# Kernel optimization log

Measured on AMD Instinct MI355X. Metric: run time of the kernel, lower is better.

## Reference

```python
import jax, jax.numpy as jnp
import numpy as np

NB, NX, NU, NY, NQ = 8192, 512, 128, 128, 256


def setup_inputs() -> dict:
    key = jax.random.key(0)
    ks = jax.random.split(key, 13)
    x = jax.random.normal(ks[0], (NB, NX), dtype=jnp.float32)
    u = jax.random.normal(ks[1], (NB, NU), dtype=jnp.float32)
    C1 = jax.random.normal(ks[2], (NQ, NX), dtype=jnp.float32) / np.sqrt(NX).astype(np.float32)
    D11 = jax.random.normal(ks[3], (NQ, NQ), dtype=jnp.float32) / np.sqrt(NQ).astype(np.float32)
    D12 = jax.random.normal(ks[4], (NQ, NU), dtype=jnp.float32) / np.sqrt(NU).astype(np.float32)
    # Lambda is a positive-diagonal matrix (only Lambda[k,k] is used in the recurrence)
    lam_diag = jax.random.uniform(ks[5], (NQ,), dtype=jnp.float32, minval=0.5, maxval=1.5)
    Lambda = jnp.diag(lam_diag)
    bv = 0.1 * jax.random.normal(ks[6], (NQ, 1), dtype=jnp.float32)
    # E must be invertible (set by the REN wrapper in the original code)
    E = jnp.eye(NX, dtype=jnp.float32) + 0.05 * jax.random.normal(ks[7], (NX, NX), dtype=jnp.float32) / np.sqrt(NX).astype(np.float32)
    F = jax.random.normal(ks[8], (NX, NX), dtype=jnp.float32) / np.sqrt(NX).astype(np.float32)
    B1 = jax.random.normal(ks[9], (NX, NQ), dtype=jnp.float32) / np.sqrt(NQ).astype(np.float32)
    B2 = jax.random.normal(ks[10], (NX, NU), dtype=jnp.float32) / np.sqrt(NU).astype(np.float32)
    C2 = jax.random.normal(ks[11], (NY, NX), dtype=jnp.float32) / np.sqrt(NX).astype(np.float32)
    D21 = jax.random.normal(ks[12], (NY, NQ), dtype=jnp.float32) / np.sqrt(NQ).astype(np.float32)
    return {"x": x, "u": u, "C1": C1, "D11": D11, "D12": D12, "Lambda": Lambda,
            "bv": bv, "E": E, "F": F, "B1": B1, "B2": B2, "C2": C2, "D21": D21}


def _solve_w(x, u, C1, D11, D12, lam_diag, bv):
    # Loop-invariant part of v_k: x @ C1[k]^T + u @ D12[k]^T + bv[k]
    base = x @ C1.T + u @ D12.T + bv[:, 0][None, :]  # (nb, nq)
    nb = x.shape[0]
    nq = C1.shape[0]

    def step(w, k):
        # w columns >= k are still zero, matching the torch loop semantics
        v = (base[:, k] + w @ D11[k]) / lam_diag[k]  # (nb,)
        w = w.at[:, k].set(jnp.tanh(v))
        return w, None

    w0 = jnp.zeros((nb, nq), dtype=x.dtype)
    w, _ = jax.lax.scan(step, w0, jnp.arange(nq))
    return w


def reference(x, u, C1, D11, D12, Lambda, bv, E, F, B1, B2, C2, D21):
    lam_diag = jnp.diagonal(Lambda)
    w = _solve_w(x, u, C1, D11, D12, lam_diag, bv)
    # E^{-1} @ M computed via solve (same math as torch.inverse(E) @ M)
    EinvF = jnp.linalg.solve(E, F)
    EinvB1 = jnp.linalg.solve(E, B1)
    EinvB2 = jnp.linalg.solve(E, B2)
    dx = x @ EinvF.T + w @ EinvB1.T + u @ EinvB2.T
    y = x @ C2.T + w @ D21.T
    return (dx, y)
```

## Files before the change

### kernel.cpp

```cpp
#include <hip/hip_runtime.h>

typedef unsigned short u16;
typedef unsigned int   u32;
typedef __attribute__((ext_vector_type(8))) __bf16 bf16x8;
typedef __attribute__((ext_vector_type(4))) float  f32x4;
typedef __attribute__((ext_vector_type(4))) u16    u16x4;
typedef __attribute__((ext_vector_type(4))) u32    u32x4;

#define DEV __device__ __forceinline__

DEV u16 f2b(float f){ union{float f;u32 u;}a; a.f=f; u32 r=a.u + 0x7FFFu + ((a.u>>16)&1u); return (u16)(r>>16); }
DEV float b2f(u16 h){ union{u32 u;float f;}a; a.u=((u32)h)<<16; return a.f; }

typedef __attribute__((address_space(1))) void* gp1;
typedef __attribute__((address_space(3))) void* lp3;
DEV void gl16(const void* g, void* l){
  __builtin_amdgcn_global_load_lds((gp1)g, (lp3)l, 16, 0, 0);
}

__global__ __launch_bounds__(256) void k_prepc(
    const float* __restrict__ x,  const float* __restrict__ u,
    const float* __restrict__ C1, const float* __restrict__ D11,
    const float* __restrict__ D12, const float* __restrict__ Lam,
    const float* __restrict__ E,  const float* __restrict__ F,
    const float* __restrict__ B1, const float* __restrict__ B2,
    const float* __restrict__ C2, const float* __restrict__ D21,
    u16* Ebf, u16* Y0, u16* Z0, u16* McatT, u16* Qt, u16* Rt,
    float* invLam, u16* Ddg2, float* Dt16, u16* P)
{
  if (blockIdx.x < 704) {
    __shared__ float t[32][33];
    int bid = blockIdx.x;
    const int tx = threadIdx.x & 31, ty = threadIdx.x >> 5;
    const float* src; u16* dst; int srcC, nA, task;
    if (bid < 256)      { task = 0; src = E;   srcC = 512; dst = Z0;    nA = 16; }
    else if (bid < 512) { task = 1; src = F;   srcC = 512; dst = McatT; nA = 16; bid -= 256; }
    else if (bid < 640) { task = 2; src = B1;  srcC = 256; dst = McatT + (size_t)640 * 512; nA = 8;  bid -= 512; }
    else                { task = 3; src = B2;  srcC = 128; dst = McatT + (size_t)512 * 512; nA = 4;  bid -= 640; }
    const int a0 = (bid % nA) * 32;
    const int b0 = (bid / nA) * 32;
    #pragma unroll
    for (int k = 0; k < 4; k++) {
      int srow = b0 + ty + 8 * k;
      t[ty + 8 * k][tx] = src[(size_t)srow * srcC + a0 + tx];
    }
    __syncthreads();
    #pragma unroll
    for (int k = 0; k < 4; k++) {
      int drow = a0 + ty + 8 * k, dcol = b0 + tx;
      float v = t[tx][ty + 8 * k];
      if (task == 0) v = ((drow == dcol) ? 2.f : 0.f) - v;
      dst[(size_t)drow * 512 + dcol] = f2b(v);
    }
    return;
  }
  int idx = (blockIdx.x - 704) * 256 + threadIdx.x;
  if (idx < 262144) {
    int i = idx >> 9, j = idx & 511;
    float e = E[idx];
    Ebf[idx] = f2b(e);
    float dij = (i == j) ? 2.f : 0.f;
    Y0[idx] = f2b(dij - e);
    return;
  }
  idx -= 262144;
  if (idx < 114688) {
    int j = idx / 896, k = idx - j * 896;
    float v = (k < 512) ? C2[j * 512 + k]
              : (k < 640 ? 0.f : D21[j * 256 + (k - 640)]);
    Qt[(size_t)(512 + j) * 896 + k] = f2b(v);
    return;
  }
  idx -= 114688;
  if (idx < 163840) {
    int n = idx / 640, k = idx - n * 640;
    float v = (k < 512) ? C1[n * 512 + k] : D12[n * 128 + (k - 512)];
    Rt[idx] = f2b(v);
    return;
  }
  idx -= 163840;
  if (idx < 256) { invLam[idx] = 1.f / Lam[idx * 257]; return; }
  idx -= 256;
  if (idx < 65536) {
    int sb = idx >> 13, t = (idx >> 9) & 15, l = (idx >> 3) & 63, j = idx & 7;
    int r = l & 15, g = l >> 4;
    int n = t * 16 + r, k = sb * 32 + g * 8 + j;
    Ddg2[idx] = f2b(D11[n * 256 + k] * (1.f / Lam[n * 257]));
    return;
  }
  idx -= 65536;
  if (idx < 4096) {
    int T = idx >> 8, k2 = (idx >> 4) & 15, n2 = idx & 15;
    float v = 0.f;
    if (n2 > k2) {
      int n = T * 16 + n2;
      v = D11[n * 256 + T * 16 + k2] * (1.f / Lam[n * 257]);
    }
    Dt16[idx] = v;
    return;
  }
  idx -= 4096;
  {
    int b = idx / 160, t = idx - b * 160;
    f32x4 s; u16* dst;
    if (t < 128) { s = *(const f32x4*)(x + (size_t)b * 512 + t * 4); dst = P + (size_t)b * 896 + t * 4; }
    else         { s = *(const f32x4*)(u + (size_t)b * 128 + (t - 128) * 4); dst = P + (size_t)b * 896 + 512 + (t - 128) * 4; }
    u16x4 o; o.x = f2b(s.x); o.y = f2b(s.y); o.z = f2b(s.z); o.w = f2b(s.w);
    *(u16x4*)dst = o;
  }
}

struct GemmArgs {
  const u16* A; const u16* B; int K; int lda; int ldb;
  u16* outB; int ldB;
  u16* outBT;
  const u16* Yprev;
};

template<int EPI>
DEV void gemm64_body(const GemmArgs& g, int bm, int bn, u16* As, u16* Bs)
{
  const int tid = threadIdx.x;
  const int l = tid & 63, w = tid >> 6;
  const int K = g.K;
  const size_t rowbA = (size_t)g.lda * 2, rowbB = (size_t)g.ldb * 2;
  const char* Ab = (const char*)g.A + (size_t)bm * 64 * rowbA;
  const char* Bb = (const char*)g.B + (size_t)bn * 64 * rowbB;
  const int o = tid * 16;
  const int r0 = o >> 6;
  const int cs = (((o >> 4) ^ r0) & 3) << 4;
  char* AsB = (char*)As; char* BsB = (char*)Bs;
  const int wm = w >> 1, wn = w & 1;
  const int lr = l & 15, lk = l >> 4;
  const int slot = ((lk ^ lr) & 3) << 4;

  f32x4 acc[2][2];
  const f32x4 zz = {0.f, 0.f, 0.f, 0.f};
  acc[0][0] = zz; acc[0][1] = zz; acc[1][0] = zz; acc[1][1] = zz;

  for (int k0 = 0; k0 < K; k0 += 32) {
    gl16(Ab + (size_t)r0 * rowbA + k0 * 2 + cs, AsB + o);
    gl16(Bb + (size_t)r0 * rowbB + k0 * 2 + cs, BsB + o);
    __syncthreads();
    bf16x8 af[2], bfv[2];
    #pragma unroll
    for (int mi = 0; mi < 2; mi++)
      af[mi] = *(const bf16x8*)(AsB + (wm * 32 + mi * 16 + lr) * 64 + slot);
    #pragma unroll
    for (int ni = 0; ni < 2; ni++)
      bfv[ni] = *(const bf16x8*)(BsB + (wn * 32 + ni * 16 + lr) * 64 + slot);
    #pragma unroll
    for (int mi = 0; mi < 2; mi++)
      #pragma unroll
      for (int ni = 0; ni < 2; ni++)
        acc[mi][ni] = __builtin_amdgcn_mfma_f32_16x16x32_bf16(af[mi], bfv[ni], acc[mi][ni], 0, 0, 0);
    __syncthreads();
  }

  #pragma unroll
  for (int mi = 0; mi < 2; mi++) {
    #pragma unroll
    for (int ni = 0; ni < 2; ni++) {
      const int row0 = bm * 64 + wm * 32 + mi * 16 + lk * 4;
      const int col  = bn * 64 + wn * 32 + ni * 16 + lr;
      if (EPI == 2) {
        #pragma unroll
        for (int r = 0; r < 4; r++)
          g.outB[(size_t)(row0 + r) * g.ldB + col] = f2b(acc[mi][ni][r]);
      } else if (EPI == 3) {
        #pragma unroll
        for (int r = 0; r < 4; r++)
          g.outBT[(size_t)col * 512 + (row0 + r)] = f2b(acc[mi][ni][r]);
      }
    }
  }
}

template<int EPI>
DEV void gemm64h_body(const GemmArgs& g, int bm, int bn, u16* As, u16* Bs)
{
  const int tid = threadIdx.x;
  const int l = tid & 63, w = tid >> 6;
  const int K = g.K;
  const size_t rowbA = (size_t)g.lda * 2, rowbB = (size_t)g.ldb * 2;
  const char* Ab = (const char*)g.A + (size_t)bm * 64 * rowbA;
  const char* Bb = (const char*)g.B + (size_t)bn * 64 * rowbB;
  const int o1 = tid * 16, o2 = o1 + 2048;
  const int rA1 = o1 >> 6, rA2 = o2 >> 6;
  const int cs1 = (((o1 >> 4) ^ rA1) & 3) << 4;
  const int cs2 = (((o2 >> 4) ^ rA2) & 3) << 4;
  char* AsB = (char*)As; char* BsB = (char*)Bs;
  const int lr = l & 15, lk = l >> 4;
  const int slot = ((lk ^ lr) & 3) << 4;

  f32x4 acc[2][4];
  const f32x4 zz = {0.f, 0.f, 0.f, 0.f};
  #pragma unroll
  for (int i = 0; i < 2; i++)
    #pragma unroll
    for (int j = 0; j < 4; j++) acc[i][j] = zz;

  for (int k0 = 0; k0 < K; k0 += 32) {
    gl16(Ab + (size_t)rA1 * rowbA + k0 * 2 + cs1, AsB + o1);
    gl16(Ab + (size_t)rA2 * rowbA + k0 * 2 + cs2, AsB + o2);
    gl16(Bb + (size_t)rA1 * rowbB + k0 * 2 + cs1, BsB + o1);
    gl16(Bb + (size_t)rA2 * rowbB + k0 * 2 + cs2, BsB + o2);
    __syncthreads();
    bf16x8 af[2], bfv[4];
    #pragma unroll
    for (int mi = 0; mi < 2; mi++)
      af[mi] = *(const bf16x8*)(AsB + (w * 32 + mi * 16 + lr) * 64 + slot);
    #pragma unroll
    for (int ni = 0; ni < 4; ni++)
      bfv[ni] = *(const bf16x8*)(BsB + (ni * 16 + lr) * 64 + slot);
    #pragma unroll
    for (int mi = 0; mi < 2; mi++)
      #pragma unroll
      for (int ni = 0; ni < 4; ni++)
        acc[mi][ni] = __builtin_amdgcn_mfma_f32_16x16x32_bf16(af[mi], bfv[ni], acc[mi][ni], 0, 0, 0);
    __syncthreads();
  }

  #pragma unroll
  for (int mi = 0; mi < 2; mi++) {
    #pragma unroll
    for (int ni = 0; ni < 4; ni++) {
      const int row0 = bm * 64 + w * 32 + mi * 16 + lk * 4;
      const int col  = bn * 64 + ni * 16 + lr;
      if (EPI == 4) {
        #pragma unroll
        for (int r = 0; r < 4; r++) {
          int row = row0 + r;
          float d = 2.f * b2f(g.Yprev[row * 512 + col]) - acc[mi][ni][r];
          g.outB[(size_t)row * 512 + col] = f2b(d);
        }
      }
    }
  }
}

template<int EPI>
__global__ __launch_bounds__(256) void gemm64(GemmArgs g)
{
  __shared__ __align__(16) u16 As[64 * 32];
  __shared__ __align__(16) u16 Bs[64 * 32];
  gemm64_body<EPI>(g, blockIdx.y, blockIdx.x, As, Bs);
}

__global__ __launch_bounds__(256) void gemm_b2(
    const u16* __restrict__ A, const u16* __restrict__ B, float* __restrict__ outF,
    const float* __restrict__ bv, const float* __restrict__ iLam, GemmArgs ga)
{
  __shared__ __align__(16) u16 As[64 * 32];
  __shared__ __align__(16) u16 Bs[128 * 32];
  if (blockIdx.x >= 256) {
    int q = blockIdx.x - 256;
    gemm64_body<3>(ga, q >> 3, q & 7, As, Bs);
    return;
  }
  const int bid = blockIdx.x;
  const int wg = (bid & 7) * 32 + (bid >> 3);
  const int bm = wg >> 1, bn = wg & 1;
  const int tid = threadIdx.x;
  const int l = tid & 63, w = tid >> 6;
  const size_t rowbA = 896 * 2, rowbB = 640 * 2;
  const char* Ab = (const char*)A + (size_t)bm * 64 * rowbA;
  const char* Bb = (const char*)B + (size_t)bn * 128 * rowbB;
  const int o = tid * 16, o2 = o + 4096;
  const int rA = o >> 6;
  const int csA = (((o >> 4) ^ rA) & 3) << 4;
  const int rB2 = o2 >> 6;
  const int csB2 = (((o2 >> 4) ^ rB2) & 3) << 4;
  char* AsB = (char*)As; char* BsB = (char*)Bs;
  const int wm = w >> 1, wn = w & 1;
  const int lr = l & 15, lk = l >> 4;
  const int slot = ((lk ^ lr) & 3) << 4;

  f32x4 acc[2][4];
  const f32x4 zz = {0.f, 0.f, 0.f, 0.f};
  #pragma unroll
  for (int i = 0; i < 2; i++)
    #pragma unroll
    for (int j = 0; j < 4; j++) acc[i][j] = zz;

  for (int k0 = 0; k0 < 640; k0 += 32) {
    gl16(Ab + (size_t)rA * rowbA + k0 * 2 + csA, AsB + o);
    gl16(Bb + (size_t)rA * rowbB + k0 * 2 + csA, BsB + o);
    gl16(Bb + (size_t)rB2 * rowbB + k0 * 2 + csB2, BsB + o2);
    __syncthreads();
    bf16x8 af[2], bfv[4];
    #pragma unroll
    for (int mi = 0; mi < 2; mi++)
      af[mi] = *(const bf16x8*)(AsB + (wm * 32 + mi * 16 + lr) * 64 + slot);
    #pragma unroll
    for (int ni = 0; ni < 4; ni++)
      bfv[ni] = *(const bf16x8*)(BsB + (wn * 64 + ni * 16 + lr) * 64 + slot);
    #pragma unroll
    for (int mi = 0; mi < 2; mi++)
      #pragma unroll
      for (int ni = 0; ni < 4; ni++)
        acc[mi][ni] = __builtin_amdgcn_mfma_f32_16x16x32_bf16(af[mi], bfv[ni], acc[mi][ni], 0, 0, 0);
    __syncthreads();
  }

  #pragma unroll
  for (int mi = 0; mi < 2; mi++) {
    #pragma unroll
    for (int ni = 0; ni < 4; ni++) {
      const int row0 = bm * 64 + wm * 32 + mi * 16 + lk * 4;
      const int col  = bn * 128 + wn * 64 + ni * 16 + lr;
      const float bvc = bv[col], il = iLam[col];
      #pragma unroll
      for (int r = 0; r < 4; r++)
        outF[(size_t)(row0 + r) * 256 + col] = (acc[mi][ni][r] + bvc) * il;
    }
  }
}

__global__ __launch_bounds__(256) void gemm_f(
    const u16* __restrict__ A, const u16* __restrict__ B,
    float* __restrict__ dxOut, float* __restrict__ yOut)
{
  __shared__ __align__(16) u16 As[128 * 32];
  __shared__ __align__(16) u16 Bs[128 * 32];
  const int bid = blockIdx.x;
  const int wg = (bid & 7) * 40 + (bid >> 3);
  const int bm = wg / 5, bn = wg - bm * 5;
  const int tid = threadIdx.x;
  const int l = tid & 63, w = tid >> 6;
  const size_t rowb = 896 * 2;
  const char* Ab = (const char*)A + (size_t)bm * 128 * rowb;
  const char* Bb = (const char*)B + (size_t)bn * 128 * rowb;
  const int o1 = tid * 16, o2 = o1 + 4096;
  const int r1 = o1 >> 6, r2 = o2 >> 6;
  const int c1 = (((o1 >> 4) ^ r1) & 3) << 4;
  const int c2 = (((o2 >> 4) ^ r2) & 3) << 4;
  char* AsB = (char*)As; char* BsB = (char*)Bs;
  const int wm = w >> 1, wn = w & 1;
  const int lr = l & 15, lk = l >> 4;
  const int slot = ((lk ^ lr) & 3) << 4;

  f32x4 acc[4][4];
  const f32x4 zz = {0.f, 0.f, 0.f, 0.f};
  #pragma unroll
  for (int i = 0; i < 4; i++)
    #pragma unroll
    for (int j = 0; j < 4; j++) acc[i][j] = zz;

  for (int k0 = 0; k0 < 896; k0 += 32) {
    gl16(Ab + (size_t)r1 * rowb + k0 * 2 + c1, AsB + o1);
    gl16(Ab + (size_t)r2 * rowb + k0 * 2 + c2, AsB + o2);
    gl16(Bb + (size_t)r1 * rowb + k0 * 2 + c1, BsB + o1);
    gl16(Bb + (size_t)r2 * rowb + k0 * 2 + c2, BsB + o2);
    __syncthreads();
    bf16x8 af[4], bfv[4];
    #pragma unroll
    for (int mi = 0; mi < 4; mi++)
      af[mi] = *(const bf16x8*)(AsB + (wm * 64 + mi * 16 + lr) * 64 + slot);
    #pragma unroll
    for (int ni = 0; ni < 4; ni++)
      bfv[ni] = *(const bf16x8*)(BsB + (wn * 64 + ni * 16 + lr) * 64 + slot);
    #pragma unroll
    for (int mi = 0; mi < 4; mi++)
      #pragma unroll
      for (int ni = 0; ni < 4; ni++)
        acc[mi][ni] = __builtin_amdgcn_mfma_f32_16x16x32_bf16(af[mi], bfv[ni], acc[mi][ni], 0, 0, 0);
    __syncthreads();
  }

  #pragma unroll
  for (int mi = 0; mi < 4; mi++) {
    #pragma unroll
    for (int ni = 0; ni < 4; ni++) {
      const int row0 = bm * 128 + wm * 64 + mi * 16 + lk * 4;
      const int col  = bn * 128 + wn * 64 + ni * 16 + lr;
      #pragma unroll
      for (int r = 0; r < 4; r++) {
        float v = acc[mi][ni][r];
        if (col < 512) dxOut[(size_t)(row0 + r) * 512 + col] = v;
        else           yOut[(size_t)(row0 + r) * 128 + (col - 512)] = v;
      }
    }
  }
}

__global__ __launch_bounds__(128) void k_solve_a(
    const float* __restrict__ base2, const u16* __restrict__ Ddg2,
    const float* __restrict__ Dt16, u16* __restrict__ P, GemmArgs ga)
{
  __shared__ __align__(16) char DdL[2][16384];
  __shared__ __align__(16) float DtL[4096];
  __shared__ __align__(16) float tb[2][16][40];

  if (blockIdx.x >= 256) {
    int q = blockIdx.x - 256;
    gemm64h_body<4>(ga, q >> 3, q & 7, (u16*)&DdL[0][0], (u16*)&DdL[0][4096]);
    return;
  }

  const int tid = threadIdx.x, l = tid & 63, w = tid >> 6;
  const int r = l & 15, g = l >> 4;
  const int row = blockIdx.x * 32 + w * 16 + r;

  const char* DtG = (const char*)Dt16;
  #pragma unroll
  for (int i = 0; i < 8; i++)
    gl16(DtG + i * 2048 + tid * 16, (char*)DtL + i * 2048 + tid * 16);
  const char* DgG = (const char*)Ddg2;
  #pragma unroll
  for (int i = 0; i < 8; i++)
    gl16(DgG + i * 2048 + tid * 16, DdL[0] + i * 2048 + tid * 16);

  f32x4 st[16];
  const float* bp = base2 + (size_t)row * 256 + g * 4;
  #pragma unroll
  for (int t = 0; t < 16; t++) st[t] = *(const f32x4*)(bp + t * 16);

  u32x4 pkA[8];
  float* tbr = &tb[w][r][0];
  __syncthreads();

  #pragma unroll
  for (int sb = 0; sb < 8; sb++) {
    if (sb < 7) {
      #pragma unroll
      for (int i = 0; i < 8; i++)
        gl16(DgG + (sb + 1) * 16384 + i * 2048 + tid * 16,
             DdL[(sb + 1) & 1] + i * 2048 + tid * 16);
    }
    float ws[8];
    #pragma unroll
    for (int i = 0; i < 8; i++) ws[i] = 0.f;
    f32x4 vv[4];

    *(f32x4*)(tbr + g * 4) = st[2 * sb];
    vv[0] = *(const f32x4*)(tbr);      vv[1] = *(const f32x4*)(tbr + 4);
    vv[2] = *(const f32x4*)(tbr + 8);  vv[3] = *(const f32x4*)(tbr + 12);
    {
      const float* dt = DtL + (2 * sb) * 256;
      #pragma unroll
      for (int k2 = 0; k2 < 16; k2++) {
        float v = vv[k2 >> 2][k2 & 3];
        float ex = __expf(2.f * v);
        float wv = 1.f - 2.f * __fdividef(1.f, ex + 1.f);
        if (g == (k2 >> 3)) ws[k2 & 7] = wv;
        #pragma unroll
        for (int j = k2 >> 2; j < 4; j++)
          vv[j] += wv * *(const f32x4*)(dt + k2 * 16 + j * 4);
      }
    }
    {
      u32x4 pk;
      pk.x = (u32)f2b(ws[0]) | ((u32)f2b(ws[1]) << 16);
      pk.y = (u32)f2b(ws[2]) | ((u32)f2b(ws[3]) << 16);
      pk.z = (u32)f2b(ws[4]) | ((u32)f2b(ws[5]) << 16);
      pk.w = (u32)f2b(ws[6]) | ((u32)f2b(ws[7]) << 16);
      union { u32x4 uu; bf16x8 bb; } cv; cv.uu = pk;
      bf16x8 Af = *(const bf16x8*)(DdL[sb & 1] + (2 * sb + 1) * 1024 + l * 16);
      st[2 * sb + 1] = __builtin_amdgcn_mfma_f32_16x16x32_bf16(Af, cv.bb, st[2 * sb + 1], 0, 0, 0);
    }
    *(f32x4*)(tbr + g * 4) = st[2 * sb + 1];
    vv[0] = *(const f32x4*)(tbr);      vv[1] = *(const f32x4*)(tbr + 4);
    vv[2] = *(const f32x4*)(tbr + 8);  vv[3] = *(const f32x4*)(tbr + 12);
    {
      const float* dt = DtL + (2 * sb + 1) * 256;
      #pragma unroll
      for (int k2 = 0; k2 < 16; k2++) {
        float v = vv[k2 >> 2][k2 & 3];
        float ex = __expf(2.f * v);
        float wv = 1.f - 2.f * __fdividef(1.f, ex + 1.f);
        if (g == 2 + (k2 >> 3)) ws[k2 & 7] = wv;
        #pragma unroll
        for (int j = k2 >> 2; j < 4; j++)
          vv[j] += wv * *(const f32x4*)(dt + k2 * 16 + j * 4);
      }
    }
    {
      u32x4 pk;
      pk.x = (u32)f2b(ws[0]) | ((u32)f2b(ws[1]) << 16);
      pk.y = (u32)f2b(ws[2]) | ((u32)f2b(ws[3]) << 16);
      pk.z = (u32)f2b(ws[4]) | ((u32)f2b(ws[5]) << 16);
      pk.w = (u32)f2b(ws[6]) | ((u32)f2b(ws[7]) << 16);
      pkA[sb] = pk;
      union { u32x4 uu; bf16x8 bb; } cv; cv.uu = pk;
      #pragma unroll
      for (int t = 0; t < 16; t++) {
        if (t >= 2 * sb + 2) {
          bf16x8 Af = *(const bf16x8*)(DdL[sb & 1] + t * 1024 + l * 16);
          st[t] = __builtin_amdgcn_mfma_f32_16x16x32_bf16(Af, cv.bb, st[t], 0, 0, 0);
        }
      }
    }
    __syncthreads();
  }

  u16* Pr = P + (size_t)row * 896 + 640;
  #pragma unroll
  for (int sb = 0; sb < 8; sb++)
    *(u32x4*)(Pr + sb * 32 + g * 8) = pkA[sb];
}

extern "C" void kernel_launch(void* const* d_in, const int* in_sizes, int n_in,
                              void* d_out, int out_size, void* d_ws, size_t ws_size,
                              hipStream_t stream)
{
  const float* x   = (const float*)d_in[0];
  const float* u   = (const float*)d_in[1];
  const float* C1  = (const float*)d_in[2];
  const float* D11 = (const float*)d_in[3];
  const float* D12 = (const float*)d_in[4];
  const float* Lam = (const float*)d_in[5];
  const float* bv  = (const float*)d_in[6];
  const float* E   = (const float*)d_in[7];
  const float* F   = (const float*)d_in[8];
  const float* B1  = (const float*)d_in[9];
  const float* B2  = (const float*)d_in[10];
  const float* C2  = (const float*)d_in[11];
  const float* D21 = (const float*)d_in[12];

  char* ws = (char*)d_ws;
  u16*   P      = (u16*)(ws);
  u16*   Qt     = (u16*)(ws + 14680064);
  u16*   Rt     = (u16*)(ws + 15826944);
  float* base2  = (float*)(ws + 16285696);
  u16*   Ddg2   = (u16*)(ws + 24674304);
  float* Dt16   = (float*)(ws + 24805376);
  u16*   Ebf    = (u16*)(ws + 24838144);
  u16*   Y0     = (u16*)(ws + 25362432);
  u16*   Z0     = (u16*)(ws + 25886720);
  u16*   T0T    = (u16*)(ws + 26411008);
  u16*   Y1     = (u16*)(ws + 26935296);
  u16*   McatT  = (u16*)(ws + 27459584);
  float* invLam = (float*)(ws + 28377088);

  float* dxOut = (float*)d_out;
  float* yOut  = dxOut + (size_t)8192 * 512;

  k_prepc<<<8209, 256, 0, stream>>>(x, u, C1, D11, D12, Lam, E, F, B1, B2, C2, D21,
                                    Ebf, Y0, Z0, McatT, Qt, Rt, invLam, Ddg2, Dt16, P);

  GemmArgs a{}; a.A = Ebf; a.B = Z0; a.K = 512; a.lda = 512; a.ldb = 512; a.outBT = T0T;
  gemm_b2<<<320, 256, 0, stream>>>(P, Rt, base2, bv, invLam, a);

  GemmArgs b{}; b.A = Y0; b.B = T0T; b.K = 512; b.lda = 512; b.ldb = 512;
  b.outB = Y1; b.ldB = 512; b.Yprev = Y0;
  k_solve_a<<<320, 128, 0, stream>>>(base2, Ddg2, Dt16, P, b);

  GemmArgs qq{}; qq.A = Y1; qq.B = McatT; qq.K = 512; qq.lda = 512; qq.ldb = 512;
  qq.outB = Qt; qq.ldB = 896;
  gemm64<2><<<dim3(14, 8), 256, 0, stream>>>(qq);

  gemm_f<<<320, 256, 0, stream>>>(P, Qt, dxOut, yOut);
  (void)in_sizes; (void)n_in; (void)out_size; (void)ws_size;
}
```

Baseline: 83.95 us.

## Fuse base GEMM into prep kernel and split final GEMM with double buffering

The base = [x u]·[C1 D12]^T GEMM moves into the prep kernel. It reads fp32 inputs directly, converts them to bf16 in registers, and applies the bias and 1/Lambda in its epilogue, which removes the separate gemm_b2 launch and the invLam buffer. The Newton-iteration GEMMs for E's inverse are reshuffled across kernels: the first runs alongside the solve, and the second runs alongside a new y-output GEMM that no longer waits for the Qt product. The final dx GEMM now uses 64-wide K tiles with double-buffered LDS and an 8-way XOR swizzle. This trades one fewer kernel launch and more overlap for longer prep-kernel blocks that do fp32 loads without async LDS copies.

```diff
diff --git a/kernel.cpp b/kernel.cpp
--- a/kernel.cpp
+++ b/kernel.cpp
@@ -17,6 +17,13 @@
 DEV void gl16(const void* g, void* l){
   __builtin_amdgcn_global_load_lds((gp1)g, (lp3)l, 16, 0, 0);
 }
+
+struct GemmArgs {
+  const u16* A; const u16* B; int K; int lda; int ldb;
+  u16* outB; int ldB;
+  u16* outBT;
+  const u16* Yprev;
+};
 
 __global__ __launch_bounds__(256) void k_prepc(
     const float* __restrict__ x,  const float* __restrict__ u,
@@ -25,12 +32,91 @@
     const float* __restrict__ E,  const float* __restrict__ F,
     const float* __restrict__ B1, const float* __restrict__ B2,
     const float* __restrict__ C2, const float* __restrict__ D21,
+    const float* __restrict__ bv,
     u16* Ebf, u16* Y0, u16* Z0, u16* McatT, u16* Qt, u16* Rt,
-    float* invLam, u16* Ddg2, float* Dt16, u16* P)
-{
-  if (blockIdx.x < 704) {
-    __shared__ float t[32][33];
-    int bid = blockIdx.x;
+    u16* Ddg2, float* Dt16, u16* P, float* base2)
+{
+  __shared__ __align__(16) char shb[8448];
+  if (blockIdx.x < 512) {
+    u16* As = (u16*)shb;
+    u16* Bs = (u16*)(shb + 4096);
+    const int q = blockIdx.x;
+    const int bm = q >> 2, bn = q & 3;
+    const int tid = threadIdx.x, l = tid & 63, w = tid >> 6;
+    const int ar = tid >> 2, acq = tid & 3;
+    const int arow = bm * 64 + ar;
+    const int bcol = bn * 64 + ar;
+    const int wm = w >> 1, wn = w & 1;
+    const int lr = l & 15, lk = l >> 4;
+    const int slot = ((lk ^ lr) & 3) << 4;
+    const int wrO = ar * 64 + (((acq ^ ar) & 3) << 4);
+
+    f32x4 acc[2][2];
+    const f32x4 zz = {0.f, 0.f, 0.f, 0.f};
+    acc[0][0] = zz; acc[0][1] = zz; acc[1][0] = zz; acc[1][1] = zz;
+
+    f32x4 a0, a1, b0, b1, na0, na1, nb0, nb1;
+    {
+      const int kk = acq * 8;
+      const float* pa = x + (size_t)arow * 512 + kk;
+      const float* pb = C1 + (size_t)bcol * 512 + kk;
+      a0 = *(const f32x4*)pa; a1 = *(const f32x4*)(pa + 4);
+      b0 = *(const f32x4*)pb; b1 = *(const f32x4*)(pb + 4);
+    }
+    for (int it = 0; it < 20; ++it) {
+      if (it < 19) {
+        const int k0 = (it + 1) * 32, kk = k0 + acq * 8;
+        const float* pa = (k0 < 512) ? (x + (size_t)arow * 512 + kk)
+                                     : (u + (size_t)arow * 128 + (kk - 512));
+        const float* pb = (k0 < 512) ? (C1 + (size_t)bcol * 512 + kk)
+                                     : (D12 + (size_t)bcol * 128 + (kk - 512));
+        na0 = *(const f32x4*)pa; na1 = *(const f32x4*)(pa + 4);
+        nb0 = *(const f32x4*)pb; nb1 = *(const f32x4*)(pb + 4);
+      }
+      u32x4 pka, pkb;
+      pka.x = (u32)f2b(a0.x) | ((u32)f2b(a0.y) << 16);
+      pka.y = (u32)f2b(a0.z) | ((u32)f2b(a0.w) << 16);
+      pka.z = (u32)f2b(a1.x) | ((u32)f2b(a1.y) << 16);
+      pka.w = (u32)f2b(a1.z) | ((u32)f2b(a1.w) << 16);
+      pkb.x = (u32)f2b(b0.x) | ((u32)f2b(b0.y) << 16);
+      pkb.y = (u32)f2b(b0.z) | ((u32)f2b(b0.w) << 16);
+      pkb.z = (u32)f2b(b1.x) | ((u32)f2b(b1.y) << 16);
+      pkb.w = (u32)f2b(b1.z) | ((u32)f2b(b1.w) << 16);
+      *(u32x4*)((char*)As + wrO) = pka;
+      *(u32x4*)((char*)Bs + wrO) = pkb;
+      __syncthreads();
+      bf16x8 af[2], bfv[2];
+      #pragma unroll
+      for (int mi = 0; mi < 2; mi++)
+        af[mi] = *(const bf16x8*)((char*)As + (wm * 32 + mi * 16 + lr) * 64 + slot);
+      #pragma unroll
+      for (int ni = 0; ni < 2; ni++)
+        bfv[ni] = *(const bf16x8*)((char*)Bs + (wn * 32 + ni * 16 + lr) * 64 + slot);
+      #pragma unroll
+      for (int mi = 0; mi < 2; mi++)
+        #pragma unroll
+        for (int ni = 0; ni < 2; ni++)
+          acc[mi][ni] = __builtin_amdgcn_mfma_f32_16x16x32_bf16(af[mi], bfv[ni], acc[mi][ni], 0, 0, 0);
+      __syncthreads();
+      a0 = na0; a1 = na1; b0 = nb0; b1 = nb1;
+    }
+    #pragma unroll
+    for (int mi = 0; mi < 2; mi++) {
+      #pragma unroll
+      for (int ni = 0; ni < 2; ni++) {
+        const int row0 = bm * 64 + wm * 32 + mi * 16 + lk * 4;
+        const int col  = bn * 64 + wn * 32 + ni * 16 + lr;
+        const float bvc = bv[col], il = 1.f / Lam[col * 257];
+        #pragma unroll
+        for (int r = 0; r < 4; r++)
+          base2[(size_t)(row0 + r) * 256 + col] = (acc[mi][ni][r] + bvc) * il;
+      }
+    }
+    return;
+  }
+  if (blockIdx.x < 1216) {
+    float (*t)[33] = (float(*)[33])shb;
+    int bid = blockIdx.x - 512;
     const int tx = threadIdx.x & 31, ty = threadIdx.x >> 5;
     const float* src; u16* dst; int srcC, nA, task;
     if (bid < 256)      { task = 0; src = E;   srcC = 512; dst = Z0;    nA = 16; }
@@ -54,7 +140,7 @@
     }
     return;
   }
-  int idx = (blockIdx.x - 704) * 256 + threadIdx.x;
+  int idx = (blockIdx.x - 1216) * 256 + threadIdx.x;
   if (idx < 262144) {
     int i = idx >> 9, j = idx & 511;
     float e = E[idx];
@@ -79,8 +165,6 @@
     return;
   }
   idx -= 163840;
-  if (idx < 256) { invLam[idx] = 1.f / Lam[idx * 257]; return; }
-  idx -= 256;
   if (idx < 65536) {
     int sb = idx >> 13, t = (idx >> 9) & 15, l = (idx >> 3) & 63, j = idx & 7;
     int r = l & 15, g = l >> 4;
@@ -109,13 +193,6 @@
     *(u16x4*)dst = o;
   }
 }
-
-struct GemmArgs {
-  const u16* A; const u16* B; int K; int lda; int ldb;
-  u16* outB; int ldB;
-  u16* outBT;
-  const u16* Yprev;
-};
 
 template<int EPI>
 DEV void gemm64_body(const GemmArgs& g, int bm, int bn, u16* As, u16* Bs)
@@ -167,13 +244,24 @@
         #pragma unroll
         for (int r = 0; r < 4; r++)
           g.outB[(size_t)(row0 + r) * g.ldB + col] = f2b(acc[mi][ni][r]);
-      } else if (EPI == 3) {
-        #pragma unroll
-        for (int r = 0; r < 4; r++)
-          g.outBT[(size_t)col * 512 + (row0 + r)] = f2b(acc[mi][ni][r]);
-      }
-    }
-  }
+      } else if (EPI == 4) {
+        #pragma unroll
+        for (int r = 0; r < 4; r++) {
+          int row = row0 + r;
+          float d = 2.f * b2f(g.Yprev[row * 512 + col]) - acc[mi][ni][r];
+          g.outB[(size_t)row * 512 + col] = f2b(d);
+        }
+      }
+    }
+  }
+}
+
+template<int EPI>
+__global__ __launch_bounds__(256) void gemm64(GemmArgs g)
+{
+  __shared__ __align__(16) u16 As[64 * 32];
+  __shared__ __align__(16) u16 Bs[64 * 32];
+  gemm64_body<EPI>(g, blockIdx.y, blockIdx.x, As, Bs);
 }
 
 template<int EPI>
@@ -227,118 +315,35 @@
     for (int ni = 0; ni < 4; ni++) {
       const int row0 = bm * 64 + w * 32 + mi * 16 + lk * 4;
       const int col  = bn * 64 + ni * 16 + lr;
-      if (EPI == 4) {
-        #pragma unroll
-        for (int r = 0; r < 4; r++) {
-          int row = row0 + r;
-          float d = 2.f * b2f(g.Yprev[row * 512 + col]) - acc[mi][ni][r];
-          g.outB[(size_t)row * 512 + col] = f2b(d);
-        }
-      }
-    }
-  }
-}
-
-template<int EPI>
-__global__ __launch_bounds__(256) void gemm64(GemmArgs g)
-{
-  __shared__ __align__(16) u16 As[64 * 32];
-  __shared__ __align__(16) u16 Bs[64 * 32];
-  gemm64_body<EPI>(g, blockIdx.y, blockIdx.x, As, Bs);
-}
-
-__global__ __launch_bounds__(256) void gemm_b2(
-    const u16* __restrict__ A, const u16* __restrict__ B, float* __restrict__ outF,
-    const float* __restrict__ bv, const float* __restrict__ iLam, GemmArgs ga)
-{
-  __shared__ __align__(16) u16 As[64 * 32];
-  __shared__ __align__(16) u16 Bs[128 * 32];
-  if (blockIdx.x >= 256) {
-    int q = blockIdx.x - 256;
-    gemm64_body<3>(ga, q >> 3, q & 7, As, Bs);
-    return;
-  }
-  const int bid = blockIdx.x;
-  const int wg = (bid & 7) * 32 + (bid >> 3);
-  const int bm = wg >> 1, bn = wg & 1;
-  const int tid = threadIdx.x;
-  const int l = tid & 63, w = tid >> 6;
-  const size_t rowbA = 896 * 2, rowbB = 640 * 2;
-  const char* Ab = (const char*)A + (size_t)bm * 64 * rowbA;
-  const char* Bb = (const char*)B + (size_t)bn * 128 * rowbB;
-  const int o = tid * 16, o2 = o + 4096;
-  const int rA = o >> 6;
-  const int csA = (((o >> 4) ^ rA) & 3) << 4;
-  const int rB2 = o2 >> 6;
-  const int csB2 = (((o2 >> 4) ^ rB2) & 3) << 4;
-  char* AsB = (char*)As; char* BsB = (char*)Bs;
-  const int wm = w >> 1, wn = w & 1;
-  const int lr = l & 15, lk = l >> 4;
-  const int slot = ((lk ^ lr) & 3) << 4;
-
-  f32x4 acc[2][4];
-  const f32x4 zz = {0.f, 0.f, 0.f, 0.f};
-  #pragma unroll
-  for (int i = 0; i < 2; i++)
-    #pragma unroll
-    for (int j = 0; j < 4; j++) acc[i][j] = zz;
-
-  for (int k0 = 0; k0 < 640; k0 += 32) {
-    gl16(Ab + (size_t)rA * rowbA + k0 * 2 + csA, AsB + o);
-    gl16(Bb + (size_t)rA * rowbB + k0 * 2 + csA, BsB + o);
-    gl16(Bb + (size_t)rB2 * rowbB + k0 * 2 + csB2, BsB + o2);
-    __syncthreads();
-    bf16x8 af[2], bfv[4];
-    #pragma unroll
-    for (int mi = 0; mi < 2; mi++)
-      af[mi] = *(const bf16x8*)(AsB + (wm * 32 + mi * 16 + lr) * 64 + slot);
-    #pragma unroll
-    for (int ni = 0; ni < 4; ni++)
-      bfv[ni] = *(const bf16x8*)(BsB + (wn * 64 + ni * 16 + lr) * 64 + slot);
-    #pragma unroll
-    for (int mi = 0; mi < 2; mi++)
-      #pragma unroll
-      for (int ni = 0; ni < 4; ni++)
-        acc[mi][ni] = __builtin_amdgcn_mfma_f32_16x16x32_bf16(af[mi], bfv[ni], acc[mi][ni], 0, 0, 0);
-    __syncthreads();
-  }
-
-  #pragma unroll
-  for (int mi = 0; mi < 2; mi++) {
-    #pragma unroll
-    for (int ni = 0; ni < 4; ni++) {
-      const int row0 = bm * 64 + wm * 32 + mi * 16 + lk * 4;
-      const int col  = bn * 128 + wn * 64 + ni * 16 + lr;
-      const float bvc = bv[col], il = iLam[col];
-      #pragma unroll
-      for (int r = 0; r < 4; r++)
-        outF[(size_t)(row0 + r) * 256 + col] = (acc[mi][ni][r] + bvc) * il;
-    }
-  }
-}
-
-__global__ __launch_bounds__(256) void gemm_f(
-    const u16* __restrict__ A, const u16* __restrict__ B,
-    float* __restrict__ dxOut, float* __restrict__ yOut)
-{
-  __shared__ __align__(16) u16 As[128 * 32];
-  __shared__ __align__(16) u16 Bs[128 * 32];
-  const int bid = blockIdx.x;
-  const int wg = (bid & 7) * 40 + (bid >> 3);
-  const int bm = wg / 5, bn = wg - bm * 5;
+      if (EPI == 3) {
+        #pragma unroll
+        for (int r = 0; r < 4; r++)
+          g.outBT[(size_t)col * 512 + (row0 + r)] = f2b(acc[mi][ni][r]);
+      }
+    }
+  }
+}
+
+template<int PART>
+DEV void f2_body(const u16* A, const u16* B, float* dxOut, float* yOut,
+                 int bm, int bn, char* sh)
+{
   const int tid = threadIdx.x;
   const int l = tid & 63, w = tid >> 6;
   const size_t rowb = 896 * 2;
   const char* Ab = (const char*)A + (size_t)bm * 128 * rowb;
   const char* Bb = (const char*)B + (size_t)bn * 128 * rowb;
-  const int o1 = tid * 16, o2 = o1 + 4096;
-  const int r1 = o1 >> 6, r2 = o2 >> 6;
-  const int c1 = (((o1 >> 4) ^ r1) & 3) << 4;
-  const int c2 = (((o2 >> 4) ^ r2) & 3) << 4;
-  char* AsB = (char*)As; char* BsB = (char*)Bs;
   const int wm = w >> 1, wn = w & 1;
   const int lr = l & 15, lk = l >> 4;
-  const int slot = ((lk ^ lr) & 3) << 4;
+
+  int oo[4]; size_t so[4];
+  #pragma unroll
+  for (int i = 0; i < 4; i++) {
+    int o = tid * 16 + i * 4096;
+    int row = o >> 7, sl = (o >> 4) & 7;
+    oo[i] = o;
+    so[i] = (size_t)row * rowb + (size_t)((sl ^ (row & 7)) << 4);
+  }
 
   f32x4 acc[4][4];
   const f32x4 zz = {0.f, 0.f, 0.f, 0.f};
@@ -347,24 +352,41 @@
     #pragma unroll
     for (int j = 0; j < 4; j++) acc[i][j] = zz;
 
-  for (int k0 = 0; k0 < 896; k0 += 32) {
-    gl16(Ab + (size_t)r1 * rowb + k0 * 2 + c1, AsB + o1);
-    gl16(Ab + (size_t)r2 * rowb + k0 * 2 + c2, AsB + o2);
-    gl16(Bb + (size_t)r1 * rowb + k0 * 2 + c1, BsB + o1);
-    gl16(Bb + (size_t)r2 * rowb + k0 * 2 + c2, BsB + o2);
-    __syncthreads();
-    bf16x8 af[4], bfv[4];
-    #pragma unroll
-    for (int mi = 0; mi < 4; mi++)
-      af[mi] = *(const bf16x8*)(AsB + (wm * 64 + mi * 16 + lr) * 64 + slot);
-    #pragma unroll
-    for (int ni = 0; ni < 4; ni++)
-      bfv[ni] = *(const bf16x8*)(BsB + (wn * 64 + ni * 16 + lr) * 64 + slot);
-    #pragma unroll
-    for (int mi = 0; mi < 4; mi++)
+  #pragma unroll
+  for (int i = 0; i < 4; i++) {
+    gl16(Ab + so[i], sh + oo[i]);
+    gl16(Bb + so[i], sh + 16384 + oo[i]);
+  }
+  __syncthreads();
+
+  for (int it = 0; it < 14; ++it) {
+    const int cur = it & 1;
+    if (it < 13) {
+      const int k0 = (it + 1) * 64;
+      char* dst = sh + ((it + 1) & 1) * 32768;
+      #pragma unroll
+      for (int i = 0; i < 4; i++) {
+        gl16(Ab + so[i] + k0 * 2, dst + oo[i]);
+        gl16(Bb + so[i] + k0 * 2, dst + 16384 + oo[i]);
+      }
+    }
+    const char* AsB = sh + cur * 32768;
+    const char* BsB = AsB + 16384;
+    #pragma unroll
+    for (int ks = 0; ks < 2; ks++) {
+      bf16x8 af[4], bfv[4];
+      #pragma unroll
+      for (int mi = 0; mi < 4; mi++)
+        af[mi] = *(const bf16x8*)(AsB + (wm * 64 + mi * 16 + lr) * 128 + (((ks * 4 + lk) ^ (lr & 7)) << 4));
       #pragma unroll
       for (int ni = 0; ni < 4; ni++)
-        acc[mi][ni] = __builtin_amdgcn_mfma_f32_16x16x32_bf16(af[mi], bfv[ni], acc[mi][ni], 0, 0, 0);
+        bfv[ni] = *(const bf16x8*)(BsB + (wn * 64 + ni * 16 + lr) * 128 + (((ks * 4 + lk) ^ (lr & 7)) << 4));
+      #pragma unroll
+      for (int mi = 0; mi < 4; mi++)
+        #pragma unroll
+        for (int ni = 0; ni < 4; ni++)
+          acc[mi][ni] = __builtin_amdgcn_mfma_f32_16x16x32_bf16(af[mi], bfv[ni], acc[mi][ni], 0, 0, 0);
+    }
     __syncthreads();
   }
 
@@ -377,11 +399,33 @@
       #pragma unroll
       for (int r = 0; r < 4; r++) {
         float v = acc[mi][ni][r];
-        if (col < 512) dxOut[(size_t)(row0 + r) * 512 + col] = v;
-        else           yOut[(size_t)(row0 + r) * 128 + (col - 512)] = v;
-      }
-    }
-  }
+        if (PART == 0) dxOut[(size_t)(row0 + r) * 512 + col] = v;
+        else           yOut[(size_t)(row0 + r) * 128 + col] = v;
+      }
+    }
+  }
+}
+
+__global__ __launch_bounds__(256) void gemm_fdx(
+    const u16* __restrict__ A, const u16* __restrict__ B, float* __restrict__ dxOut)
+{
+  __shared__ __align__(16) char sh[65536];
+  const int bid = blockIdx.x;
+  const int wg = (bid & 7) * 32 + (bid >> 3);
+  f2_body<0>(A, B, dxOut, nullptr, wg >> 2, wg & 3, sh);
+}
+
+__global__ __launch_bounds__(256) void k_l3(
+    const u16* __restrict__ P, const u16* __restrict__ QtY,
+    float* __restrict__ yOut, GemmArgs gy1)
+{
+  __shared__ __align__(16) char sh[65536];
+  if (blockIdx.x < 64) {
+    f2_body<1>(P, QtY, nullptr, yOut, blockIdx.x, 0, sh);
+    return;
+  }
+  int q = blockIdx.x - 64;
+  gemm64_body<4>(gy1, q >> 3, q & 7, (u16*)sh, (u16*)(sh + 4096));
 }
 
 __global__ __launch_bounds__(128) void k_solve_a(
@@ -394,7 +438,7 @@
 
   if (blockIdx.x >= 256) {
     int q = blockIdx.x - 256;
-    gemm64h_body<4>(ga, q >> 3, q & 7, (u16*)&DdL[0][0], (u16*)&DdL[0][4096]);
+    gemm64h_body<3>(ga, q >> 3, q & 7, (u16*)&DdL[0][0], (u16*)&DdL[0][4096]);
     return;
   }
 
@@ -531,25 +575,24 @@
   u16*   T0T    = (u16*)(ws + 26411008);
   u16*   Y1     = (u16*)(ws + 26935296);
   u16*   McatT  = (u16*)(ws + 27459584);
-  float* invLam = (float*)(ws + 28377088);
 
   float* dxOut = (float*)d_out;
   float* yOut  = dxOut + (size_t)8192 * 512;
 
-  k_prepc<<<8209, 256, 0, stream>>>(x, u, C1, D11, D12, Lam, E, F, B1, B2, C2, D21,
-                                    Ebf, Y0, Z0, McatT, Qt, Rt, invLam, Ddg2, Dt16, P);
+  k_prepc<<<8720, 256, 0, stream>>>(x, u, C1, D11, D12, Lam, E, F, B1, B2, C2, D21,
+                                    bv, Ebf, Y0, Z0, McatT, Qt, Rt, Ddg2, Dt16, P, base2);
 
   GemmArgs a{}; a.A = Ebf; a.B = Z0; a.K = 512; a.lda = 512; a.ldb = 512; a.outBT = T0T;
-  gemm_b2<<<320, 256, 0, stream>>>(P, Rt, base2, bv, invLam, a);
+  k_solve_a<<<320, 128, 0, stream>>>(base2, Ddg2, Dt16, P, a);
 
   GemmArgs b{}; b.A = Y0; b.B = T0T; b.K = 512; b.lda = 512; b.ldb = 512;
   b.outB = Y1; b.ldB = 512; b.Yprev = Y0;
-  k_solve_a<<<320, 128, 0, stream>>>(base2, Ddg2, Dt16, P, b);
+  k_l3<<<128, 256, 0, stream>>>(P, Qt + (size_t)512 * 896, yOut, b);
 
   GemmArgs qq{}; qq.A = Y1; qq.B = McatT; qq.K = 512; qq.lda = 512; qq.ldb = 512;
   qq.outB = Qt; qq.ldB = 896;
   gemm64<2><<<dim3(14, 8), 256, 0, stream>>>(qq);
 
-  gemm_f<<<320, 256, 0, stream>>>(P, Qt, dxOut, yOut);
+  gemm_fdx<<<256, 256, 0, stream>>>(P, Qt, dxOut);
   (void)in_sizes; (void)n_in; (void)out_size; (void)ws_size;
 }
```

New measurement: 89.87 us. +7.0%, slower.

## Split final GEMM and run y-output part alongside the Qt GEMM

Applied to the files above, without the earlier changes.

The final fused GEMM that wrote both dx and y is split in two. The y-part, which reads rows of Qt that do not depend on the Y1 chain, now runs as 64 extra blocks inside the same launch as the 112-block Qt-producing GEMM, so an under-filled launch gets more work. The remaining dx GEMM launches 256 blocks instead of 320. This shortens the critical path after Qt is ready, at the cost of a mixed-role kernel with a shared LDS buffer and an assumption that the y rows of Qt are ready before that launch.

```diff
diff --git a/kernel.cpp b/kernel.cpp
--- a/kernel.cpp
+++ b/kernel.cpp
@@ -17,6 +17,13 @@
 DEV void gl16(const void* g, void* l){
   __builtin_amdgcn_global_load_lds((gp1)g, (lp3)l, 16, 0, 0);
 }
+
+struct GemmArgs {
+  const u16* A; const u16* B; int K; int lda; int ldb;
+  u16* outB; int ldB;
+  u16* outBT;
+  const u16* Yprev;
+};
 
 __global__ __launch_bounds__(256) void k_prepc(
     const float* __restrict__ x,  const float* __restrict__ u,
@@ -109,13 +116,6 @@
     *(u16x4*)dst = o;
   }
 }
-
-struct GemmArgs {
-  const u16* A; const u16* B; int K; int lda; int ldb;
-  u16* outB; int ldB;
-  u16* outBT;
-  const u16* Yprev;
-};
 
 template<int EPI>
 DEV void gemm64_body(const GemmArgs& g, int bm, int bn, u16* As, u16* Bs)
@@ -237,14 +237,6 @@
       }
     }
   }
-}
-
-template<int EPI>
-__global__ __launch_bounds__(256) void gemm64(GemmArgs g)
-{
-  __shared__ __align__(16) u16 As[64 * 32];
-  __shared__ __align__(16) u16 Bs[64 * 32];
-  gemm64_body<EPI>(g, blockIdx.y, blockIdx.x, As, Bs);
 }
 
 __global__ __launch_bounds__(256) void gemm_b2(
@@ -317,15 +309,12 @@
   }
 }
 
-__global__ __launch_bounds__(256) void gemm_f(
-    const u16* __restrict__ A, const u16* __restrict__ B,
-    float* __restrict__ dxOut, float* __restrict__ yOut)
-{
-  __shared__ __align__(16) u16 As[128 * 32];
-  __shared__ __align__(16) u16 Bs[128 * 32];
-  const int bid = blockIdx.x;
-  const int wg = (bid & 7) * 40 + (bid >> 3);
-  const int bm = wg / 5, bn = wg - bm * 5;
+template<int PART>
+DEV void f2_body(const u16* A, const u16* B, float* dxOut, float* yOut,
+                 int bm, int bn, char* sh)
+{
+  char* AsB = sh;
+  char* BsB = sh + 8192;
   const int tid = threadIdx.x;
   const int l = tid & 63, w = tid >> 6;
   const size_t rowb = 896 * 2;
@@ -335,7 +324,6 @@
   const int r1 = o1 >> 6, r2 = o2 >> 6;
   const int c1 = (((o1 >> 4) ^ r1) & 3) << 4;
   const int c2 = (((o2 >> 4) ^ r2) & 3) << 4;
-  char* AsB = (char*)As; char* BsB = (char*)Bs;
   const int wm = w >> 1, wn = w & 1;
   const int lr = l & 15, lk = l >> 4;
   const int slot = ((lk ^ lr) & 3) << 4;
@@ -377,11 +365,34 @@
       #pragma unroll
       for (int r = 0; r < 4; r++) {
         float v = acc[mi][ni][r];
-        if (col < 512) dxOut[(size_t)(row0 + r) * 512 + col] = v;
-        else           yOut[(size_t)(row0 + r) * 128 + (col - 512)] = v;
+        if (PART == 0) dxOut[(size_t)(row0 + r) * 512 + col] = v;
+        else           yOut[(size_t)(row0 + r) * 128 + col] = v;
       }
     }
   }
+}
+
+__global__ __launch_bounds__(256) void k_l4(
+    const u16* __restrict__ P, const u16* __restrict__ QtY,
+    float* __restrict__ yOut, GemmArgs qt)
+{
+  __shared__ __align__(16) char sh[16384];
+  if (blockIdx.x < 64) {
+    const int bm = (blockIdx.x & 7) * 8 + (blockIdx.x >> 3);
+    f2_body<1>(P, QtY, nullptr, yOut, bm, 0, sh);
+    return;
+  }
+  int q = blockIdx.x - 64;
+  gemm64_body<2>(qt, q / 14, q % 14, (u16*)sh, (u16*)(sh + 4096));
+}
+
+__global__ __launch_bounds__(256) void gemm_fdx(
+    const u16* __restrict__ A, const u16* __restrict__ B, float* __restrict__ dxOut)
+{
+  __shared__ __align__(16) char sh[16384];
+  const int bid = blockIdx.x;
+  const int wg = (bid & 7) * 32 + (bid >> 3);
+  f2_body<0>(A, B, dxOut, nullptr, wg >> 2, wg & 3, sh);
 }
 
 __global__ __launch_bounds__(128) void k_solve_a(
@@ -548,8 +559,8 @@
 
   GemmArgs qq{}; qq.A = Y1; qq.B = McatT; qq.K = 512; qq.lda = 512; qq.ldb = 512;
   qq.outB = Qt; qq.ldB = 896;
-  gemm64<2><<<dim3(14, 8), 256, 0, stream>>>(qq);
-
-  gemm_f<<<320, 256, 0, stream>>>(P, Qt, dxOut, yOut);
+  k_l4<<<176, 256, 0, stream>>>(P, Qt + (size_t)512 * 896, yOut, qq);
+
+  gemm_fdx<<<256, 256, 0, stream>>>(P, Qt, dxOut);
   (void)in_sizes; (void)n_in; (void)out_size; (void)ws_size;
 }
```

Result: slower. 94.16 us (+12.1%).
